# Performance work log

Measured on AMD Instinct MI355X. Metric: run time of the kernel, lower is better.

The kernel has to match this reference:

```python
import jax, jax.numpy as jnp
import numpy as np

B, C, L, D, E, K = 64, 23, 26000, 64, 512, 3  # batch, chromosomes, bins/chr, d_model, eos_dim, num_states
V = C * L


def setup_inputs() -> dict:
    key = jax.random.key(0)
    k0, k1, k2, k3 = jax.random.split(key, 4)
    return {
        "eos_emb": jax.random.normal(k0, (B, C, E), jnp.float32),
        "bin_ids": jnp.arange(C * L, dtype=jnp.int32).reshape(C, L),
        "emb_table": jax.random.normal(k1, (V, D), jnp.float32) * 0.02,
        "eos_W": jax.random.normal(k2, (D, E), jnp.float32) / np.float32(np.sqrt(E)),
        "eos_b": jnp.zeros((D,), jnp.float32),
        "fc_W": jax.random.normal(k3, (K, 2 * D), jnp.float32) / np.float32(np.sqrt(2 * D)),
        "fc_b": jnp.zeros((K,), jnp.float32),
    }


def reference(eos_emb, bin_ids, emb_table, eos_W, eos_b, fc_W, fc_b):
    # eos_projection (use_eos_proj=True): [B,C,E] @ [D,E]^T + b -> [B,C,D]
    eos = jnp.einsum('bce,de->bcd', eos_emb, eos_W) + eos_b
    # per-chromosome embedding gather (bin_projection skipped: bin_emb_dim == d_model, use_bin_proj=False)
    bin_emb = emb_table[bin_ids]  # [C,L,D]
    # fc on concat([bin, eos]) == bin @ Wb^T + eos @ We^T + b (avoids materializing [B,C,L,2D])
    Wb, We = fc_W[:, :D], fc_W[:, D:]
    a = jnp.einsum('cld,kd->clk', bin_emb, Wb)          # [C,L,K]
    e = jnp.einsum('bcd,kd->bck', eos, We) + fc_b       # [B,C,K]
    return jax.nn.relu(a[None, :, :, :] + e[:, :, None, :])  # [B,C,L,K]
```

## Files before the change

kernel.cpp:

```cpp
#include <hip/hip_runtime.h>

#define NB 64
#define NC 23
#define NL 26000
#define ND 64
#define NE 512
#define NK 3

__global__ __launch_bounds__(64) void eos_e_kernel(
    const float* __restrict__ eos_emb,
    const float* __restrict__ eos_W,
    const float* __restrict__ eos_b,
    const float* __restrict__ fc_W,
    const float* __restrict__ fc_b,
    float* __restrict__ e_out)
{
    const int bc = blockIdx.x;
    const int d  = threadIdx.x;

    __shared__ float xs[NE];
    float4* xs4 = reinterpret_cast<float4*>(xs);
    const float4* src = reinterpret_cast<const float4*>(eos_emb + (size_t)bc * NE);
    for (int i = d; i < NE / 4; i += 64) xs4[i] = src[i];
    __syncthreads();

    const float4* wrow = reinterpret_cast<const float4*>(eos_W + (size_t)d * NE);
    float acc = 0.f;
    #pragma unroll 8
    for (int i = 0; i < NE / 4; ++i) {
        float4 w = wrow[i];
        float4 x = xs4[i];
        acc += w.x * x.x;
        acc += w.y * x.y;
        acc += w.z * x.z;
        acc += w.w * x.w;
    }
    const float eosd = acc + eos_b[d];

    #pragma unroll
    for (int k = 0; k < NK; ++k) {
        float p = eosd * fc_W[k * (2 * ND) + ND + d];
        #pragma unroll
        for (int off = 32; off > 0; off >>= 1) p += __shfl_xor(p, off, 64);
        if (d == 0) e_out[(size_t)bc * NK + k] = p + fc_b[k];
    }
}

__global__ __launch_bounds__(256) void decoder_main_kernel(
    const int*   __restrict__ bin_ids,
    const float* __restrict__ emb_table,
    const float* __restrict__ fc_W,
    const float* __restrict__ e_in,
    float* __restrict__ out)
{
    const int c   = blockIdx.y;
    const int tid = threadIdx.x;
    const int l   = blockIdx.x * 256 + tid;

    __shared__ float wb[NK][ND];
    __shared__ float es[NB * NK];

    if (tid < NK * ND)
        wb[tid / ND][tid % ND] = fc_W[(tid / ND) * (2 * ND) + (tid % ND)];
    if (tid < NB * NK) {
        int b = tid / NK, k = tid % NK;
        es[tid] = e_in[((size_t)b * NC + c) * NK + k];
    }
    __syncthreads();
    if (l >= NL) return;

    const int row = bin_ids[(size_t)c * NL + l];
    const float4* er = reinterpret_cast<const float4*>(emb_table + (size_t)row * ND);
    const float4* w0 = reinterpret_cast<const float4*>(wb[0]);
    const float4* w1 = reinterpret_cast<const float4*>(wb[1]);
    const float4* w2 = reinterpret_cast<const float4*>(wb[2]);

    float a0 = 0.f, a1 = 0.f, a2 = 0.f;
    #pragma unroll
    for (int i = 0; i < ND / 4; ++i) {
        float4 v  = er[i];
        float4 p0 = w0[i], p1 = w1[i], p2 = w2[i];
        a0 += v.x * p0.x + v.y * p0.y + v.z * p0.z + v.w * p0.w;
        a1 += v.x * p1.x + v.y * p1.y + v.z * p1.z + v.w * p1.w;
        a2 += v.x * p2.x + v.y * p2.y + v.z * p2.z + v.w * p2.w;
    }

    size_t obase = ((size_t)c * NL + l) * NK;
    const size_t bstride = (size_t)NC * NL * NK;
    #pragma unroll 4
    for (int b = 0; b < NB; ++b) {
        const float e0 = es[b * NK + 0];
        const float e1 = es[b * NK + 1];
        const float e2 = es[b * NK + 2];
        out[obase + 0] = fmaxf(a0 + e0, 0.f);
        out[obase + 1] = fmaxf(a1 + e1, 0.f);
        out[obase + 2] = fmaxf(a2 + e2, 0.f);
        obase += bstride;
    }
}

extern "C" void kernel_launch(void* const* d_in, const int* in_sizes, int n_in,
                              void* d_out, int out_size, void* d_ws, size_t ws_size,
                              hipStream_t stream) {
    const float* eos_emb   = (const float*)d_in[0];
    const int*   bin_ids   = (const int*)  d_in[1];
    const float* emb_table = (const float*)d_in[2];
    const float* eos_W     = (const float*)d_in[3];
    const float* eos_b     = (const float*)d_in[4];
    const float* fc_W      = (const float*)d_in[5];
    const float* fc_b      = (const float*)d_in[6];
    float*       out       = (float*)d_out;
    float*       e_ws      = (float*)d_ws;

    eos_e_kernel<<<NB * NC, 64, 0, stream>>>(eos_emb, eos_W, eos_b, fc_W, fc_b, e_ws);

    dim3 grid((NL + 255) / 256, NC);
    decoder_main_kernel<<<grid, 256, 0, stream>>>(bin_ids, emb_table, fc_W, e_ws, out);
}
```

Measured before the change: 171.7 us.

## Split decoder into separate a-projection and broadcast-store kernels via workspace

```diff
diff --git a/kernel.cpp b/kernel.cpp
--- a/kernel.cpp
+++ b/kernel.cpp
@@ -46,7 +46,77 @@
     }
 }
 
-__global__ __launch_bounds__(256) void decoder_main_kernel(
+__global__ __launch_bounds__(256) void a_kernel(
+    const int*   __restrict__ bin_ids,
+    const float* __restrict__ emb_table,
+    const float* __restrict__ fc_W,
+    float* __restrict__ a_out)
+{
+    const int c   = blockIdx.y;
+    const int tid = threadIdx.x;
+    const int l   = blockIdx.x * 256 + tid;
+
+    __shared__ float wb[NK][ND];
+    if (tid < NK * ND)
+        wb[tid / ND][tid % ND] = fc_W[(tid / ND) * (2 * ND) + (tid % ND)];
+    __syncthreads();
+    if (l >= NL) return;
+
+    const int row = bin_ids[(size_t)c * NL + l];
+    const float4* er = reinterpret_cast<const float4*>(emb_table + (size_t)row * ND);
+    const float4* w0 = reinterpret_cast<const float4*>(wb[0]);
+    const float4* w1 = reinterpret_cast<const float4*>(wb[1]);
+    const float4* w2 = reinterpret_cast<const float4*>(wb[2]);
+
+    float a0 = 0.f, a1 = 0.f, a2 = 0.f;
+    #pragma unroll
+    for (int i = 0; i < ND / 4; ++i) {
+        float4 v  = er[i];
+        float4 p0 = w0[i], p1 = w1[i], p2 = w2[i];
+        a0 += v.x * p0.x + v.y * p0.y + v.z * p0.z + v.w * p0.w;
+        a1 += v.x * p1.x + v.y * p1.y + v.z * p1.z + v.w * p1.w;
+        a2 += v.x * p2.x + v.y * p2.y + v.z * p2.z + v.w * p2.w;
+    }
+
+    float* dst = a_out + ((size_t)c * NL + l) * NK;
+    dst[0] = a0; dst[1] = a1; dst[2] = a2;
+}
+
+__global__ __launch_bounds__(256) void store_kernel(
+    const float* __restrict__ a_in,
+    const float* __restrict__ e_in,
+    float* __restrict__ out)
+{
+    const int c   = blockIdx.y;
+    const int tid = threadIdx.x;
+    const int l   = blockIdx.x * 256 + tid;
+
+    __shared__ float es[NB * NK];
+    if (tid < NB * NK) {
+        int b = tid / NK, k = tid % NK;
+        es[tid] = e_in[((size_t)b * NC + c) * NK + k];
+    }
+    __syncthreads();
+    if (l >= NL) return;
+
+    const float* ap = a_in + ((size_t)c * NL + l) * NK;
+    const float a0 = ap[0], a1 = ap[1], a2 = ap[2];
+
+    size_t obase = ((size_t)c * NL + l) * NK;
+    const size_t bstride = (size_t)NC * NL * NK;
+    #pragma unroll 8
+    for (int b = 0; b < NB; ++b) {
+        const float e0 = es[b * NK + 0];
+        const float e1 = es[b * NK + 1];
+        const float e2 = es[b * NK + 2];
+        out[obase + 0] = fmaxf(a0 + e0, 0.f);
+        out[obase + 1] = fmaxf(a1 + e1, 0.f);
+        out[obase + 2] = fmaxf(a2 + e2, 0.f);
+        obase += bstride;
+    }
+}
+
+__global__ __launch_bounds__(256) void decoder_fused_kernel(
     const int*   __restrict__ bin_ids,
     const float* __restrict__ emb_table,
     const float* __restrict__ fc_W,
@@ -110,10 +180,19 @@
     const float* fc_W      = (const float*)d_in[5];
     const float* fc_b      = (const float*)d_in[6];
     float*       out       = (float*)d_out;
-    float*       e_ws      = (float*)d_ws;
+
+    float*  e_ws = (float*)d_ws;
+    const size_t a_off_bytes = 32768;
+    float*  a_ws = (float*)((char*)d_ws + a_off_bytes);
+    const size_t a_bytes = (size_t)NC * NL * NK * sizeof(float);
 
     eos_e_kernel<<<NB * NC, 64, 0, stream>>>(eos_emb, eos_W, eos_b, fc_W, fc_b, e_ws);
 
     dim3 grid((NL + 255) / 256, NC);
-    decoder_main_kernel<<<grid, 256, 0, stream>>>(bin_ids, emb_table, fc_W, e_ws, out);
+    if (ws_size >= a_off_bytes + a_bytes) {
+        a_kernel<<<grid, 256, 0, stream>>>(bin_ids, emb_table, fc_W, a_ws);
+        store_kernel<<<grid, 256, 0, stream>>>(a_ws, e_ws, out);
+    } else {
+        decoder_fused_kernel<<<grid, 256, 0, stream>>>(bin_ids, emb_table, fc_W, e_ws, out);
+    }
 }
```

Result: slower. 175.1 us (+2.0%).
